# Kernel optimization log

Hardware: AMD Instinct MI355X
Metric: run time of the kernel (lower is better)

Reference implementation:

```python
import jax, jax.numpy as jnp
import numpy as np

B, S, D = 8, 1024, 1152
H, HD = 16, 72  # num_heads, head_dim

def setup_inputs() -> dict:
    key = jax.random.key(0)
    ks = jax.random.split(key, 7)
    hidden_states = jax.random.normal(ks[0], (B, S, D), dtype=jnp.float32)
    cos = jax.random.uniform(ks[1], (S, HD), dtype=jnp.float32)
    sin = jax.random.uniform(ks[2], (S, HD), dtype=jnp.float32)
    qkv_w = jax.random.normal(ks[3], (3 * D, D), dtype=jnp.float32) * 0.02
    qkv_b = jnp.zeros((3 * D,), dtype=jnp.float32)
    proj_w = jax.random.normal(ks[4], (D, D), dtype=jnp.float32) * 0.02
    proj_b = jnp.zeros((D,), dtype=jnp.float32)
    return {"hidden_states": hidden_states, "cos": cos, "sin": sin,
            "qkv_w": qkv_w, "qkv_b": qkv_b, "proj_w": proj_w, "proj_b": proj_b}

def _rotate_half(x):
    x1, x2 = jnp.split(x, 2, axis=-1)
    return jnp.concatenate((-x2, x1), axis=-1)

def reference(hidden_states, cos, sin, qkv_w, qkv_b, proj_w, proj_b):
    b, s, d = hidden_states.shape
    # fused QKV projection
    qkv = hidden_states @ qkv_w.T + qkv_b            # [B,S,3D]
    qkv = qkv.reshape(b, s, 3, H, HD)
    qkv = jnp.transpose(qkv, (2, 0, 3, 1, 4))        # [3,B,H,S,HD]
    q, k, v = qkv[0], qkv[1], qkv[2]
    # rotary embedding, cos/sin broadcast [1,1,S,HD]
    c = cos[None, None, :, :]
    sn = sin[None, None, :, :]
    q = q * c + _rotate_half(q) * sn
    k = k * c + _rotate_half(k) * sn
    # SDPA
    scale = HD ** -0.5
    scores = jnp.einsum('bhqd,bhkd->bhqk', q, k) * scale
    probs = jax.nn.softmax(scores, axis=-1)
    attn = jnp.einsum('bhqk,bhkd->bhqd', probs, v)   # [B,H,S,HD]
    attn = jnp.transpose(attn, (0, 2, 1, 3)).reshape(b, s, d)
    return attn @ proj_w.T + proj_b
```

## Files before the change

### kernel.cpp

```cpp
#include <hip/hip_runtime.h>
#include <hip/hip_bf16.h>


typedef __attribute__((ext_vector_type(8))) short short8;
typedef __attribute__((ext_vector_type(4))) float f32x4;

__device__ __forceinline__ float bflo(unsigned int u) { return __uint_as_float(u << 16); }

__device__ __forceinline__ unsigned int f2bf(float f) {
    unsigned int u = __float_as_uint(f);
    return (u + 0x7FFFu + ((u >> 16) & 1u)) >> 16;
}

__device__ __forceinline__ void stout(float* C, size_t idx, float v) { C[idx] = v; }
__device__ __forceinline__ void stout(__hip_bfloat16* C, size_t idx, float v) {
    C[idx] = __float2bfloat16(v);
}

__device__ __forceinline__ void async_cp16(const void* g, void* l) {
    __builtin_amdgcn_global_load_lds((const __attribute__((address_space(1))) void*)g,
                                     (__attribute__((address_space(3))) void*)l, 16, 0, 0);
}

__global__ void f32_to_bf16_pair(
    const float* __restrict__ s0, unsigned short* __restrict__ d0, int n0_4,
    const float* __restrict__ s1, unsigned short* __restrict__ d1, int n1_4)
{
    int i = blockIdx.x * 256 + threadIdx.x;
    const float* s; unsigned short* d;
    if (i < n0_4) { s = s0; d = d0; }
    else if (i < n0_4 + n1_4) { s = s1; d = d1; i -= n0_4; }
    else return;
    float4 f = ((const float4*)s)[i];
    ushort4 r;
    r.x = (unsigned short)f2bf(f.x);
    r.y = (unsigned short)f2bf(f.y);
    r.z = (unsigned short)f2bf(f.z);
    r.w = (unsigned short)f2bf(f.w);
    ((ushort4*)d)[i] = r;
}

template <typename OT>
__global__ __launch_bounds__(256, 2) void gemm_bt_lds(
    const __hip_bfloat16* __restrict__ A,
    const __hip_bfloat16* __restrict__ B,
    const float* __restrict__ bias,
    OT* __restrict__ C,
    int M, int N, int K)
{
    __shared__ __align__(16) unsigned short As[2 * 128 * 32];
    __shared__ __align__(16) unsigned short Bs[2 * 128 * 32];

    const int tid  = threadIdx.x;
    const int lane = tid & 63;
    const int w    = tid >> 6;
    const int wr   = w >> 1;
    const int wc   = w & 1;
    const int bm   = blockIdx.y * 128;
    const int bn   = blockIdx.x * 128;

    const int lrow = lane >> 2;
    const int lcol = (lane & 3) * 8;

    const unsigned short* ag[4];
    const unsigned short* bg[4];
    unsigned short* al[4];
    unsigned short* bl[4];
#pragma unroll
    for (int c = 0; c < 2; c++) {
        const int r = w * 32 + c * 16 + lrow;
#pragma unroll
        for (int h = 0; h < 2; h++) {
            const int idx = c * 2 + h;
            ag[idx] = (const unsigned short*)A + (size_t)(bm + r) * K + h * 32 + lcol;
            bg[idx] = (const unsigned short*)B + (size_t)(bn + r) * K + h * 32 + lcol;
            al[idx] = &As[h * 4096 + (w * 2 + c) * 512];
            bl[idx] = &Bs[h * 4096 + (w * 2 + c) * 512];
        }
    }

    f32x4 acc[4][4];
#pragma unroll
    for (int i = 0; i < 4; i++)
#pragma unroll
        for (int j = 0; j < 4; j++)
            acc[i][j] = (f32x4){0.f, 0.f, 0.f, 0.f};

    const int kq = (lane >> 4) * 8;
    const int fr = lane & 15;

    for (int k0 = 0; k0 < K; k0 += 64) {
        __syncthreads();
#pragma unroll
        for (int c = 0; c < 4; c++) {
            async_cp16(ag[c] + k0, al[c]);
            async_cp16(bg[c] + k0, bl[c]);
        }
        __syncthreads();

#pragma unroll
        for (int h = 0; h < 2; h++) {
            short8 af[4], bf[4];
#pragma unroll
            for (int i = 0; i < 4; i++)
                af[i] = *(const short8*)&As[h * 4096 + (wr * 64 + i * 16 + fr) * 32 + kq];
#pragma unroll
            for (int j = 0; j < 4; j++)
                bf[j] = *(const short8*)&Bs[h * 4096 + (wc * 64 + j * 16 + fr) * 32 + kq];
#pragma unroll
            for (int i = 0; i < 4; i++)
#pragma unroll
                for (int j = 0; j < 4; j++)
                    acc[i][j] = __builtin_amdgcn_mfma_f32_16x16x32_bf16(af[i], bf[j], acc[i][j], 0, 0, 0);
        }
    }

#pragma unroll
    for (int i = 0; i < 4; i++) {
        const int mrow = bm + wr * 64 + i * 16 + (lane >> 4) * 4;
#pragma unroll
        for (int j = 0; j < 4; j++) {
            const int ncol = bn + wc * 64 + j * 16 + fr;
            const float bv = bias[ncol];
#pragma unroll
            for (int r = 0; r < 4; r++) {
                stout(C, (size_t)(mrow + r) * N + ncol, acc[i][j][r] + bv);
            }
        }
    }
}

__global__ void rope_v_prep(
    const __hip_bfloat16* __restrict__ qkv,
    const float* __restrict__ cosp,
    const float* __restrict__ sinp,
    __hip_bfloat16* __restrict__ Qo,
    __hip_bfloat16* __restrict__ Ko,
    __hip_bfloat16* __restrict__ Vt)
{
    __shared__ __align__(16) unsigned short T[64 * 72];
    const int tid = threadIdx.x;
    const int bh = blockIdx.x >> 4;
    const int st = blockIdx.x & 15;
    const int b = bh >> 4, h = bh & 15;
    const size_t row0 = ((size_t)b * 1024 + st * 64) * 3456;

    const unsigned short* vsrc = (const unsigned short*)qkv + row0 + 2304 + h * 72;
#pragma unroll
    for (int k = 0; k < 3; k++) {
        const int c = tid + k * 256;
        if (c < 576) {
            const int s = c / 9, off = (c % 9) * 8;
            *(uint4*)&T[c * 8] = *(const uint4*)(vsrc + (size_t)s * 3456 + off);
        }
    }

    const unsigned short* qkvp = (const unsigned short*)qkv;
    const float QS = 0.17002324f;
#pragma unroll
    for (int k = 0; k < 9; k++) {
        const int p = tid + k * 256;
        const int sl = p / 36, i = p % 36;
        const int sg = st * 64 + sl;
        const size_t row = row0 + (size_t)sl * 3456;
        const int col = h * 72 + i;

        const float c1 = cosp[sg * 72 + i];
        const float c2 = cosp[sg * 72 + i + 36];
        const float s1 = sinp[sg * 72 + i];
        const float s2 = sinp[sg * 72 + i + 36];

        const float qa = bflo((unsigned int)qkvp[row + col] << 16 >> 16 | ((unsigned int)qkvp[row + col]));
        const float qa2 = __uint_as_float((unsigned int)qkvp[row + col] << 16);
        const float qb  = __uint_as_float((unsigned int)qkvp[row + col + 36] << 16);
        const float ka  = __uint_as_float((unsigned int)qkvp[row + 1152 + col] << 16);
        const float kb  = __uint_as_float((unsigned int)qkvp[row + 1152 + col + 36] << 16);
        (void)qa;

        const size_t ob = ((size_t)bh * 1024 + sg) * 72 + i;
        ((unsigned short*)Qo)[ob]      = (unsigned short)f2bf((qa2 * c1 - qb * s1) * QS);
        ((unsigned short*)Qo)[ob + 36] = (unsigned short)f2bf((qb * c2 + qa2 * s2) * QS);
        ((unsigned short*)Ko)[ob]      = (unsigned short)f2bf(ka * c1 - kb * s1);
        ((unsigned short*)Ko)[ob + 36] = (unsigned short)f2bf(kb * c2 + ka * s2);
    }

    __syncthreads();

    unsigned short* dst = (unsigned short*)Vt + (size_t)(bh * 16 + st) * 72 * 64;
#pragma unroll
    for (int k = 0; k < 9; k++) {
        const int o = tid + k * 256;
        const int d = o >> 5;
        const int sl = (o & 31) * 2;
        ushort2 v;
        v.x = T[sl * 72 + d];
        v.y = T[(sl + 1) * 72 + d];
        *(ushort2*)&dst[d * 64 + sl] = v;
    }
}

__global__ __launch_bounds__(256, 4) void attn_mfma(
    const __hip_bfloat16* __restrict__ Q,
    const __hip_bfloat16* __restrict__ K,
    const __hip_bfloat16* __restrict__ Vt,
    __hip_bfloat16* __restrict__ O)
{
    __shared__ __align__(16) unsigned short Ks[64][72];
    __shared__ __align__(16) unsigned short Vs[80][72];
    __shared__ __align__(16) unsigned short Ps[4][32][72];

    const int tid  = threadIdx.x;
    const int lane = tid & 63;
    const int w    = tid >> 6;
    const int quad = lane >> 4;
    const int fr   = lane & 15;
    const int bh   = blockIdx.x & 127;
    const int qt   = blockIdx.x >> 7;
    const int qbase = qt * 128 + w * 32;

    const short8 z8 = (short8){0,0,0,0,0,0,0,0};

    for (int idx = tid; idx < 8 * 72; idx += 256)
        Vs[72 + idx / 72][idx % 72] = (idx < 72) ? (unsigned short)0x3F80 : (unsigned short)0;

    const unsigned short* qp = (const unsigned short*)Q + ((size_t)bh * 1024 + qbase + fr) * 72;
    short8 qf[2][3];
#pragma unroll
    for (int sub = 0; sub < 2; sub++) {
        const unsigned short* qs = qp + sub * 16 * 72;
        qf[sub][0] = *(const short8*)(qs + quad * 8);
        qf[sub][1] = *(const short8*)(qs + 32 + quad * 8);
        qf[sub][2] = (quad == 0) ? *(const short8*)(qs + 64) : z8;
    }

    f32x4 Oa[2][5];
#pragma unroll
    for (int sub = 0; sub < 2; sub++)
#pragma unroll
        for (int n = 0; n < 5; n++) Oa[sub][n] = (f32x4){0.f, 0.f, 0.f, 0.f};

    const unsigned short* kg0 = (const unsigned short*)K + (size_t)bh * 1024 * 72;
    const unsigned short* vg0 = (const unsigned short*)Vt + (size_t)bh * 16 * 72 * 64;

#pragma unroll 1
    for (int t = 0; t < 16; t++) {
        __syncthreads();
        const unsigned short* kg = kg0 + (size_t)t * 64 * 72;
        const unsigned short* vg = vg0 + (size_t)t * 72 * 64;
#pragma unroll
        for (int k = 0; k < 3; k++) {
            const int c = tid + k * 256;
            if (c < 576) {
                *(uint4*)&((unsigned short*)Ks)[c * 8] = *(const uint4*)(kg + c * 8);
                *(uint4*)&Vs[c >> 3][(c & 7) * 8] = *(const uint4*)(vg + c * 8);
            }
        }
        __syncthreads();

#pragma unroll
        for (int nt = 0; nt < 4; nt++) {
            short8 b0 = *(const short8*)&Ks[nt * 16 + fr][quad * 8];
            short8 b1 = *(const short8*)&Ks[nt * 16 + fr][32 + quad * 8];
            short8 b2 = (quad == 0) ? *(const short8*)&Ks[nt * 16 + fr][64] : z8;
            f32x4 s0 = (f32x4){0.f, 0.f, 0.f, 0.f};
            f32x4 s1 = (f32x4){0.f, 0.f, 0.f, 0.f};
            s0 = __builtin_amdgcn_mfma_f32_16x16x32_bf16(qf[0][0], b0, s0, 0, 0, 0);
            s1 = __builtin_amdgcn_mfma_f32_16x16x32_bf16(qf[1][0], b0, s1, 0, 0, 0);
            s0 = __builtin_amdgcn_mfma_f32_16x16x32_bf16(qf[0][1], b1, s0, 0, 0, 0);
            s1 = __builtin_amdgcn_mfma_f32_16x16x32_bf16(qf[1][1], b1, s1, 0, 0, 0);
            s0 = __builtin_amdgcn_mfma_f32_16x16x32_bf16(qf[0][2], b2, s0, 0, 0, 0);
            s1 = __builtin_amdgcn_mfma_f32_16x16x32_bf16(qf[1][2], b2, s1, 0, 0, 0);
#pragma unroll
            for (int r = 0; r < 4; r++) {
                Ps[w][quad * 4 + r][nt * 16 + fr]      = (unsigned short)f2bf(exp2f(s0[r]));
                Ps[w][16 + quad * 4 + r][nt * 16 + fr] = (unsigned short)f2bf(exp2f(s1[r]));
            }
        }

#pragma unroll
        for (int ks = 0; ks < 2; ks++) {
            short8 ap0 = *(const short8*)&Ps[w][fr][ks * 32 + quad * 8];
            short8 ap1 = *(const short8*)&Ps[w][16 + fr][ks * 32 + quad * 8];
#pragma unroll
            for (int n = 0; n < 5; n++) {
                short8 bv = *(const short8*)&Vs[n * 16 + fr][ks * 32 + quad * 8];
                Oa[0][n] = __builtin_amdgcn_mfma_f32_16x16x32_bf16(ap0, bv, Oa[0][n], 0, 0, 0);
                Oa[1][n] = __builtin_amdgcn_mfma_f32_16x16x32_bf16(ap1, bv, Oa[1][n], 0, 0, 0);
            }
        }
    }

    const int lsrc = (lane & 48) | 8;
    const int b = bh >> 4, h = bh & 15;
    unsigned short* ob = (unsigned short*)O;
#pragma unroll
    for (int sub = 0; sub < 2; sub++) {
        float inv[4];
#pragma unroll
        for (int r = 0; r < 4; r++)
            inv[r] = 1.f / __shfl(Oa[sub][4][r], lsrc, 64);
#pragma unroll
        for (int n = 0; n < 5; n++) {
            const int d = n * 16 + fr;
            if (d < 72) {
#pragma unroll
                for (int r = 0; r < 4; r++) {
                    const size_t idx =
                        ((size_t)b * 1024 + qbase + sub * 16 + quad * 4 + r) * 1152 + h * 72 + d;
                    ob[idx] = (unsigned short)f2bf(Oa[sub][n][r] * inv[r]);
                }
            }
        }
    }
}

extern "C" void kernel_launch(void* const* d_in, const int* in_sizes, int n_in,
                              void* d_out, int out_size, void* d_ws, size_t ws_size,
                              hipStream_t stream)
{
    const float* hs     = (const float*)d_in[0];
    const float* cosp   = (const float*)d_in[1];
    const float* sinp   = (const float*)d_in[2];
    const float* qkv_w  = (const float*)d_in[3];
    const float* qkv_b  = (const float*)d_in[4];
    const float* proj_w = (const float*)d_in[5];
    const float* proj_b = (const float*)d_in[6];
    float* out = (float*)d_out;

    char* ws = (char*)d_ws;
    __hip_bfloat16* qkv_buf = (__hip_bfloat16*)ws;
    __hip_bfloat16* Qb = (__hip_bfloat16*)(ws + 56623104);
    __hip_bfloat16* Kb = Qb + 9437184;
    __hip_bfloat16* Vt = Kb + 9437184;
    __hip_bfloat16* Ab = qkv_buf;

    unsigned short* hs_bf = (unsigned short*)Qb;
    unsigned short* qw_bf = (unsigned short*)Kb;
    unsigned short* pw_bf = (unsigned short*)Qb;

    f32_to_bf16_pair<<<13104, 256, 0, stream>>>(hs, hs_bf, 2359296,
                                                qkv_w, qw_bf, 995328);
    gemm_bt_lds<__hip_bfloat16>
        <<<dim3(27, 64), 256, 0, stream>>>((const __hip_bfloat16*)hs_bf,
                                           (const __hip_bfloat16*)qw_bf,
                                           qkv_b, qkv_buf, 8192, 3456, 1152);
    rope_v_prep<<<2048, 256, 0, stream>>>(qkv_buf, cosp, sinp, Qb, Kb, Vt);
    attn_mfma<<<1024, 256, 0, stream>>>(Qb, Kb, Vt, Ab);
    f32_to_bf16_pair<<<1296, 256, 0, stream>>>(proj_w, pw_bf, 331776,
                                               nullptr, nullptr, 0);
    gemm_bt_lds<float>
        <<<dim3(9, 64), 256, 0, stream>>>((const __hip_bfloat16*)Ab,
                                          (const __hip_bfloat16*)pw_bf,
                                          proj_b, out, 8192, 1152, 1152);
}
```

Measured before the change: 339.5 us.

## Replace GEMM with 256x256-tile, 8-wave, ping-pong pipelined LDS kernel with swizzled layout

```diff
diff --git a/kernel.cpp b/kernel.cpp
--- a/kernel.cpp
+++ b/kernel.cpp
@@ -4,8 +4,6 @@
 
 typedef __attribute__((ext_vector_type(8))) short short8;
 typedef __attribute__((ext_vector_type(4))) float f32x4;
-
-__device__ __forceinline__ float bflo(unsigned int u) { return __uint_as_float(u << 16); }
 
 __device__ __forceinline__ unsigned int f2bf(float f) {
     unsigned int u = __float_as_uint(f);
@@ -24,107 +22,219 @@
 
 __global__ void f32_to_bf16_pair(
     const float* __restrict__ s0, unsigned short* __restrict__ d0, int n0_4,
-    const float* __restrict__ s1, unsigned short* __restrict__ d1, int n1_4)
+    const float* __restrict__ s1, unsigned short* __restrict__ d1, int n1_4,
+    unsigned short* __restrict__ dz, int nz_4)
 {
     int i = blockIdx.x * 256 + threadIdx.x;
-    const float* s; unsigned short* d;
-    if (i < n0_4) { s = s0; d = d0; }
-    else if (i < n0_4 + n1_4) { s = s1; d = d1; i -= n0_4; }
-    else return;
-    float4 f = ((const float4*)s)[i];
-    ushort4 r;
-    r.x = (unsigned short)f2bf(f.x);
-    r.y = (unsigned short)f2bf(f.y);
-    r.z = (unsigned short)f2bf(f.z);
-    r.w = (unsigned short)f2bf(f.w);
-    ((ushort4*)d)[i] = r;
-}
+    if (i < n0_4) {
+        float4 f = ((const float4*)s0)[i];
+        ushort4 r;
+        r.x = (unsigned short)f2bf(f.x);
+        r.y = (unsigned short)f2bf(f.y);
+        r.z = (unsigned short)f2bf(f.z);
+        r.w = (unsigned short)f2bf(f.w);
+        ((ushort4*)d0)[i] = r;
+        return;
+    }
+    i -= n0_4;
+    if (i < n1_4) {
+        float4 f = ((const float4*)s1)[i];
+        ushort4 r;
+        r.x = (unsigned short)f2bf(f.x);
+        r.y = (unsigned short)f2bf(f.y);
+        r.z = (unsigned short)f2bf(f.z);
+        r.w = (unsigned short)f2bf(f.w);
+        ((ushort4*)d1)[i] = r;
+        return;
+    }
+    i -= n1_4;
+    if (i < nz_4) {
+        ushort4 z; z.x = 0; z.y = 0; z.z = 0; z.w = 0;
+        ((ushort4*)dz)[i] = z;
+    }
+}
+
+template <int ISB, int H>
+__device__ __forceinline__ void stage_ht(const unsigned short* __restrict__ g, int ldg,
+                                         int k0, unsigned short* l, int w, int lane)
+{
+#pragma unroll
+    for (int t = 0; t < 2; t++) {
+        const int c  = w * 2 + t;
+        const int r0 = ISB ? ((c >> 2) * 64 + H * 32 + (c & 3) * 8)
+                           : ((c & 8) * 16 + H * 64 + (c & 7) * 8);
+        const int rl = r0 + (lane >> 3);
+        const int gg = (lane & 7) ^ (lane >> 3);
+        async_cp16(g + (size_t)rl * ldg + k0 + gg * 8, l + r0 * 64);
+    }
+}
+
+#define LDA(MH, SRC)                                                              \
+    _Pragma("unroll") for (int mi = 0; mi < 4; ++mi) {                            \
+        Af[mi][0] = *(const short8*)((SRC) + aRow + (MH) * 4096 + mi * 1024 + g0); \
+        Af[mi][1] = *(const short8*)((SRC) + aRow + (MH) * 4096 + mi * 1024 + g1); \
+    }
+
+#define LDB(DST, NH, SRC)                                                         \
+    _Pragma("unroll") for (int ni = 0; ni < 2; ++ni) {                            \
+        DST[ni][0] = *(const short8*)((SRC) + bRow + (NH) * 2048 + ni * 1024 + g0); \
+        DST[ni][1] = *(const short8*)((SRC) + bRow + (NH) * 2048 + ni * 1024 + g1); \
+    }
+
+#define MFMAS(MH, NH, PB)                                                         \
+    __builtin_amdgcn_s_setprio(1);                                                \
+    _Pragma("unroll") for (int mi = 0; mi < 4; ++mi)                              \
+    _Pragma("unroll") for (int ni = 0; ni < 2; ++ni) {                            \
+        acc[(MH) * 4 + mi][(NH) * 2 + ni] = __builtin_amdgcn_mfma_f32_16x16x32_bf16( \
+            Af[mi][0], PB[ni][0], acc[(MH) * 4 + mi][(NH) * 2 + ni], 0, 0, 0);    \
+        acc[(MH) * 4 + mi][(NH) * 2 + ni] = __builtin_amdgcn_mfma_f32_16x16x32_bf16( \
+            Af[mi][1], PB[ni][1], acc[(MH) * 4 + mi][(NH) * 2 + ni], 0, 0, 0);    \
+    }                                                                             \
+    __builtin_amdgcn_s_setprio(0);
+
+#define MIDBAR()                                                   \
+    do {                                                           \
+        __builtin_amdgcn_s_barrier();                              \
+        asm volatile("s_waitcnt lgkmcnt(0)" ::: "memory");         \
+        __builtin_amdgcn_sched_barrier(0);                         \
+    } while (0)
+
+#define ENDBAR()                                                   \
+    do {                                                           \
+        __builtin_amdgcn_s_barrier();                              \
+        __builtin_amdgcn_sched_barrier(0);                         \
+    } while (0)
 
 template <typename OT>
-__global__ __launch_bounds__(256, 2) void gemm_bt_lds(
-    const __hip_bfloat16* __restrict__ A,
-    const __hip_bfloat16* __restrict__ B,
+__global__ __launch_bounds__(512, 2) void gemm_bt_256(
+    const __hip_bfloat16* __restrict__ Abf,
+    const __hip_bfloat16* __restrict__ Bbf,
     const float* __restrict__ bias,
     OT* __restrict__ C,
-    int M, int N, int K)
-{
-    __shared__ __align__(16) unsigned short As[2 * 128 * 32];
-    __shared__ __align__(16) unsigned short Bs[2 * 128 * 32];
+    int M, int Nreal, int K)
+{
+    __shared__ __align__(16) unsigned short smem[2][2][256 * 64];
 
     const int tid  = threadIdx.x;
     const int lane = tid & 63;
     const int w    = tid >> 6;
-    const int wr   = w >> 1;
-    const int wc   = w & 1;
-    const int bm   = blockIdx.y * 128;
-    const int bn   = blockIdx.x * 128;
-
-    const int lrow = lane >> 2;
-    const int lcol = (lane & 3) * 8;
-
-    const unsigned short* ag[4];
-    const unsigned short* bg[4];
-    unsigned short* al[4];
-    unsigned short* bl[4];
-#pragma unroll
-    for (int c = 0; c < 2; c++) {
-        const int r = w * 32 + c * 16 + lrow;
-#pragma unroll
-        for (int h = 0; h < 2; h++) {
-            const int idx = c * 2 + h;
-            ag[idx] = (const unsigned short*)A + (size_t)(bm + r) * K + h * 32 + lcol;
-            bg[idx] = (const unsigned short*)B + (size_t)(bn + r) * K + h * 32 + lcol;
-            al[idx] = &As[h * 4096 + (w * 2 + c) * 512];
-            bl[idx] = &Bs[h * 4096 + (w * 2 + c) * 512];
-        }
-    }
-
-    f32x4 acc[4][4];
-#pragma unroll
-    for (int i = 0; i < 4; i++)
-#pragma unroll
-        for (int j = 0; j < 4; j++)
-            acc[i][j] = (f32x4){0.f, 0.f, 0.f, 0.f};
-
-    const int kq = (lane >> 4) * 8;
-    const int fr = lane & 15;
-
-    for (int k0 = 0; k0 < K; k0 += 64) {
-        __syncthreads();
-#pragma unroll
-        for (int c = 0; c < 4; c++) {
-            async_cp16(ag[c] + k0, al[c]);
-            async_cp16(bg[c] + k0, bl[c]);
-        }
-        __syncthreads();
-
-#pragma unroll
-        for (int h = 0; h < 2; h++) {
-            short8 af[4], bf[4];
-#pragma unroll
-            for (int i = 0; i < 4; i++)
-                af[i] = *(const short8*)&As[h * 4096 + (wr * 64 + i * 16 + fr) * 32 + kq];
-#pragma unroll
-            for (int j = 0; j < 4; j++)
-                bf[j] = *(const short8*)&Bs[h * 4096 + (wc * 64 + j * 16 + fr) * 32 + kq];
-#pragma unroll
-            for (int i = 0; i < 4; i++)
-#pragma unroll
-                for (int j = 0; j < 4; j++)
-                    acc[i][j] = __builtin_amdgcn_mfma_f32_16x16x32_bf16(af[i], bf[j], acc[i][j], 0, 0, 0);
-        }
-    }
-
-#pragma unroll
-    for (int i = 0; i < 4; i++) {
-        const int mrow = bm + wr * 64 + i * 16 + (lane >> 4) * 4;
-#pragma unroll
-        for (int j = 0; j < 4; j++) {
-            const int ncol = bn + wc * 64 + j * 16 + fr;
-            const float bv = bias[ncol];
-#pragma unroll
-            for (int r = 0; r < 4; r++) {
-                stout(C, (size_t)(mrow + r) * N + ncol, acc[i][j][r] + bv);
+    const int wm   = w >> 2;
+    const int wn   = w & 3;
+    const int q    = lane >> 4;
+    const int fr   = lane & 15;
+    const int xr   = fr & 7;
+
+    const int nwg = gridDim.x * gridDim.y;
+    const int lin = blockIdx.y * gridDim.x + blockIdx.x;
+    const int swz = (lin & 7) * (nwg >> 3) + (lin >> 3);
+    const int bn  = (swz % gridDim.x) * 256;
+    const int bm  = (swz / gridDim.x) * 256;
+
+    const unsigned short* Ag = (const unsigned short*)Abf + (size_t)bm * K;
+    const unsigned short* Bg = (const unsigned short*)Bbf + (size_t)bn * K;
+
+    unsigned short* s00 = &smem[0][0][0];
+    unsigned short* s01 = &smem[0][1][0];
+    unsigned short* s10 = &smem[1][0][0];
+    unsigned short* s11 = &smem[1][1][0];
+
+    const int NT = K >> 6;
+    const int NI = NT >> 1;
+
+    const int aRow = (wm * 128 + fr) * 64;
+    const int bRow = (wn * 64 + fr) * 64;
+    const int g0   = ((0 * 4 + q) ^ xr) * 8;
+    const int g1   = ((1 * 4 + q) ^ xr) * 8;
+
+    f32x4 acc[8][4];
+#pragma unroll
+    for (int i = 0; i < 8; i++)
+#pragma unroll
+        for (int j = 0; j < 4; j++) acc[i][j] = (f32x4){0.f, 0.f, 0.f, 0.f};
+
+    short8 Af[4][2], Bf0[2][2], Bf1[2][2];
+
+    stage_ht<0, 0>(Ag, K, 0, s00, w, lane);
+    stage_ht<0, 1>(Ag, K, 0, s00, w, lane);
+    stage_ht<1, 0>(Bg, K, 0, s01, w, lane);
+    stage_ht<1, 1>(Bg, K, 0, s01, w, lane);
+    stage_ht<0, 0>(Ag, K, 64, s10, w, lane);
+    stage_ht<1, 1>(Bg, K, 64, s10 + 16384, w, lane);
+    stage_ht<0, 1>(Ag, K, 64, s10, w, lane);
+    asm volatile("s_waitcnt vmcnt(6)" ::: "memory");
+    ENDBAR();
+
+#pragma unroll 1
+    for (int i = 0; i < NI; i++) {
+        const int k1 = (2 * i + 1) * 64;
+        const int t2 = 2 * i + 2, t3 = 2 * i + 3;
+        const int k2 = (t2 < NT ? t2 : NT - 1) * 64;
+        const int k3 = (t3 < NT ? t3 : NT - 1) * 64;
+
+        LDA(0, s00);
+        LDB(Bf0, 0, s01);
+        stage_ht<1, 0>(Bg, K, k1, s11, w, lane);
+        asm volatile("s_waitcnt lgkmcnt(8)" ::: "memory");
+        MIDBAR();
+        MFMAS(0, 0, Bf0);
+        ENDBAR();
+
+        LDB(Bf1, 1, s01);
+        stage_ht<0, 0>(Ag, K, k2, s00, w, lane);
+        MIDBAR();
+        MFMAS(0, 1, Bf1);
+        ENDBAR();
+
+        LDA(1, s00);
+        stage_ht<1, 1>(Bg, K, k2, s01, w, lane);
+        MIDBAR();
+        MFMAS(1, 1, Bf1);
+        ENDBAR();
+
+        stage_ht<0, 1>(Ag, K, k2, s00, w, lane);
+        asm volatile("s_waitcnt vmcnt(6)" ::: "memory");
+        MIDBAR();
+        MFMAS(1, 0, Bf0);
+        ENDBAR();
+
+        LDA(0, s10);
+        LDB(Bf0, 0, s11);
+        stage_ht<1, 0>(Bg, K, k2, s01, w, lane);
+        asm volatile("s_waitcnt lgkmcnt(8)" ::: "memory");
+        MIDBAR();
+        MFMAS(0, 0, Bf0);
+        ENDBAR();
+
+        LDB(Bf1, 1, s11);
+        stage_ht<0, 0>(Ag, K, k3, s10, w, lane);
+        MIDBAR();
+        MFMAS(0, 1, Bf1);
+        ENDBAR();
+
+        LDA(1, s10);
+        stage_ht<1, 1>(Bg, K, k3, s11, w, lane);
+        MIDBAR();
+        MFMAS(1, 1, Bf1);
+        ENDBAR();
+
+        stage_ht<0, 1>(Ag, K, k3, s10, w, lane);
+        asm volatile("s_waitcnt vmcnt(6)" ::: "memory");
+        MIDBAR();
+        MFMAS(1, 0, Bf0);
+        ENDBAR();
+    }
+
+#pragma unroll
+    for (int mf = 0; mf < 8; mf++) {
+        const int row = bm + wm * 128 + mf * 16 + q * 4;
+#pragma unroll
+        for (int nf = 0; nf < 4; nf++) {
+            const int col = bn + wn * 64 + nf * 16 + fr;
+            if (col < Nreal) {
+                const float bv = bias[col];
+#pragma unroll
+                for (int r = 0; r < 4; r++)
+                    stout(C, (size_t)(row + r) * Nreal + col, acc[mf][nf][r] + bv);
             }
         }
     }
@@ -170,16 +280,14 @@
         const float s1 = sinp[sg * 72 + i];
         const float s2 = sinp[sg * 72 + i + 36];
 
-        const float qa = bflo((unsigned int)qkvp[row + col] << 16 >> 16 | ((unsigned int)qkvp[row + col]));
-        const float qa2 = __uint_as_float((unsigned int)qkvp[row + col] << 16);
-        const float qb  = __uint_as_float((unsigned int)qkvp[row + col + 36] << 16);
-        const float ka  = __uint_as_float((unsigned int)qkvp[row + 1152 + col] << 16);
-        const float kb  = __uint_as_float((unsigned int)qkvp[row + 1152 + col + 36] << 16);
-        (void)qa;
+        const float qa = __uint_as_float((unsigned int)qkvp[row + col] << 16);
+        const float qb = __uint_as_float((unsigned int)qkvp[row + col + 36] << 16);
+        const float ka = __uint_as_float((unsigned int)qkvp[row + 1152 + col] << 16);
+        const float kb = __uint_as_float((unsigned int)qkvp[row + 1152 + col + 36] << 16);
 
         const size_t ob = ((size_t)bh * 1024 + sg) * 72 + i;
-        ((unsigned short*)Qo)[ob]      = (unsigned short)f2bf((qa2 * c1 - qb * s1) * QS);
-        ((unsigned short*)Qo)[ob + 36] = (unsigned short)f2bf((qb * c2 + qa2 * s2) * QS);
+        ((unsigned short*)Qo)[ob]      = (unsigned short)f2bf((qa * c1 - qb * s1) * QS);
+        ((unsigned short*)Qo)[ob + 36] = (unsigned short)f2bf((qb * c2 + qa * s2) * QS);
         ((unsigned short*)Ko)[ob]      = (unsigned short)f2bf(ka * c1 - kb * s1);
         ((unsigned short*)Ko)[ob + 36] = (unsigned short)f2bf(kb * c2 + ka * s2);
     }
@@ -338,18 +446,20 @@
     unsigned short* qw_bf = (unsigned short*)Kb;
     unsigned short* pw_bf = (unsigned short*)Qb;
 
-    f32_to_bf16_pair<<<13104, 256, 0, stream>>>(hs, hs_bf, 2359296,
-                                                qkv_w, qw_bf, 995328);
-    gemm_bt_lds<__hip_bfloat16>
-        <<<dim3(27, 64), 256, 0, stream>>>((const __hip_bfloat16*)hs_bf,
+    f32_to_bf16_pair<<<13248, 256, 0, stream>>>(hs, hs_bf, 2359296,
+                                                qkv_w, qw_bf, 995328,
+                                                qw_bf + 3981312, 36864);
+    gemm_bt_256<__hip_bfloat16>
+        <<<dim3(14, 32), 512, 0, stream>>>((const __hip_bfloat16*)hs_bf,
                                            (const __hip_bfloat16*)qw_bf,
                                            qkv_b, qkv_buf, 8192, 3456, 1152);
     rope_v_prep<<<2048, 256, 0, stream>>>(qkv_buf, cosp, sinp, Qb, Kb, Vt);
     attn_mfma<<<1024, 256, 0, stream>>>(Qb, Kb, Vt, Ab);
-    f32_to_bf16_pair<<<1296, 256, 0, stream>>>(proj_w, pw_bf, 331776,
-                                               nullptr, nullptr, 0);
-    gemm_bt_lds<float>
-        <<<dim3(9, 64), 256, 0, stream>>>((const __hip_bfloat16*)Ab,
+    f32_to_bf16_pair<<<1440, 256, 0, stream>>>(proj_w, pw_bf, 331776,
+                                               nullptr, nullptr, 0,
+                                               pw_bf + 1327104, 36864);
+    gemm_bt_256<float>
+        <<<dim3(5, 32), 512, 0, stream>>>((const __hip_bfloat16*)Ab,
                                           (const __hip_bfloat16*)pw_bf,
                                           proj_b, out, 8192, 1152, 1152);
 }
```

New measurement: 312.7 us. 1.09x faster.
